# Performance work log

Measured on AMD Instinct MI355X. Metric: run time of the kernel, lower is better.

Reference implementation:

```python
import jax, jax.numpy as jnp
import numpy as np

EPS = 1e-12  # F.normalize default eps


def setup_inputs() -> dict:
    key = jax.random.key(0)
    k1, k2 = jax.random.split(key)
    b, c, angRes, h, w = 4, 64, 5, 64, 64
    d = 64  # dims
    x = jax.random.normal(k1, (b, c, angRes * angRes, h, w), dtype=jnp.float32)
    # 1x1 conv weight [3*dims, channels] (kernel size 1, no bias)
    W = jax.random.normal(k2, (3 * d, c), dtype=jnp.float32) * 0.02
    return {"x": x, "W": W}


def reference(x, W):
    b, c, n, h, w = x.shape
    d = W.shape[0] // 3
    # 1x1 conv over angular (u,v) grid == channel matmul; rearranges are free reindexings
    qkv = jnp.einsum('oc,bcnhw->bonhw', W, x)  # [b, 3d, n, h, w]
    q, k, v = jnp.split(qkv, 3, axis=1)        # each [b, d, n, h, w]

    def flat(t):  # '(b h w) c u v -> b (u v) (c h w)'
        return t.transpose(0, 2, 1, 3, 4).reshape(b, n, d * h * w)

    q, k, v = flat(q), flat(k), flat(v)
    # L2-normalize along the (c h w) feature dim (k was normalized on dim=-2 of its
    # transposed layout, which is this same feature dim)
    q = q / jnp.maximum(jnp.linalg.norm(q, axis=-1, keepdims=True), EPS)
    k = k / jnp.maximum(jnp.linalg.norm(k, axis=-1, keepdims=True), EPS)
    att = jax.nn.softmax(jnp.einsum('bnf,bmf->bnm', q, k), axis=-1)  # [b, n, n], n=25
    out = jnp.einsum('bnm,bmf->bnf', att, v)   # [b, n, d*h*w]
    # 'b (u v) (c h w) -> b c (u v) h w'
    return out.reshape(b, n, d, h, w).transpose(0, 2, 1, 3, 4)
```

## Files before the change

### kernel.cpp

```cpp
#include <hip/hip_runtime.h>

#define B   4
#define C   64
#define D   64
#define NN  25
#define HW  4096
#define F   (D*HW)

#define PT  128
#define QCH 256
#define NCH 4

typedef unsigned short ushort_t;
typedef unsigned int   uint_t;
typedef __attribute__((ext_vector_type(8)))  short  short8;
typedef __attribute__((ext_vector_type(8)))  unsigned short us8;
typedef __attribute__((ext_vector_type(16))) float  floatx16;
typedef __attribute__((ext_vector_type(4)))  float  f32x4;
typedef __attribute__((ext_vector_type(4)))  unsigned short us4;

__device__ ushort_t g_Wthi[128 * C];
__device__ ushort_t g_Wtlo[128 * C];
__device__ ushort_t g_Wvhi[D * C];
__device__ ushort_t g_Wvlo[D * C];

__device__ float g_S[B * NN * NN];
__device__ float g_qq[B * NN];
__device__ float g_kk[B * NN];
__device__ float g_attT[B * NN * NN];

static __device__ __forceinline__ ushort_t f2bf(float f) {
    uint_t u = __float_as_uint(f);
    u += 0x7FFFu + ((u >> 16) & 1u);
    return (ushort_t)(u >> 16);
}
static __device__ __forceinline__ float bf2f(ushort_t h) {
    return __uint_as_float((uint_t)h << 16);
}

static __device__ __forceinline__ int lds_x(int p, int c) {
    return p * 64 + ((((c >> 3) ^ (p & 7)) << 3) | (c & 7));
}

__global__ void k_zero() {
    int i = blockIdx.x * 256 + threadIdx.x;
    if (i < 2500)      g_S[i] = 0.f;
    else if (i < 2600) g_qq[i - 2500] = 0.f;
    else if (i < 2700) g_kk[i - 2600] = 0.f;
}

__global__ void k_wprep(const float* __restrict__ W) {
    int i = blockIdx.x * 256 + threadIdx.x;
    if (i < 128 * 64) {
        float w = W[i];
        ushort_t hi = f2bf(w);
        g_Wthi[i] = hi;
        g_Wtlo[i] = f2bf(w - bf2f(hi));
    } else if (i < 192 * 64) {
        float w = W[i];
        int j = i - 128 * 64;
        ushort_t hi = f2bf(w);
        g_Wvhi[j] = hi;
        g_Wvlo[j] = f2bf(w - bf2f(hi));
    }
}

__global__ void __launch_bounds__(256, 4)
k_proj(const float* __restrict__ x,
       ushort_t* __restrict__ Q, ushort_t* __restrict__ K,
       float* __restrict__ V) {
    __shared__ ushort_t sXhi[PT * 64];
    __shared__ ushort_t sXlo[PT * 64];

    const int t  = threadIdx.x;
    const int wv = t >> 6, ln = t & 63;
    const int n  = blockIdx.y, b = blockIdx.z;
    const int tile = blockIdx.x;
    const int gp0  = tile * PT;

    const int row = ln & 31, kh = (ln >> 5) * 8, d0 = wv * 32;
    short8 ahi[4], alo[4];
#pragma unroll
    for (int ks = 0; ks < 4; ++ks) {
        ahi[ks] = *(const short8*)&g_Wthi[(d0 + row) * 64 + ks * 16 + kh];
        alo[ks] = *(const short8*)&g_Wtlo[(d0 + row) * 64 + ks * 16 + kh];
    }

    {
        const int c16 = wv * 16;
#pragma unroll
        for (int cg = 0; cg < 4; ++cg) {
            const int c4 = c16 + cg * 4;
            const float* xc = x + ((size_t)(b * C + c4) * NN + n) * HW + gp0;
#pragma unroll
            for (int ph = 0; ph < 2; ++ph) {
                const int p = ph * 64 + ln;
                float v[4];
#pragma unroll
                for (int i = 0; i < 4; ++i) v[i] = xc[(size_t)i * NN * HW + p];
                us4 h, l;
#pragma unroll
                for (int i = 0; i < 4; ++i) {
                    ushort_t hi = f2bf(v[i]);
                    h[i] = hi;
                    l[i] = f2bf(v[i] - bf2f(hi));
                }
                *(us4*)&sXhi[lds_x(p, c4)] = h;
                *(us4*)&sXlo[lds_x(p, c4)] = l;
            }
        }
    }
    __syncthreads();

    ushort_t* __restrict__ O = (wv < 2) ? Q : K;
    const int slab = (wv < 2) ? wv : wv - 2;
    const size_t nbase = (size_t)(b * NN + n) * F;

    float nrm = 0.f;
#pragma unroll
    for (int pt = 0; pt < 4; ++pt) {
        const int pcol = pt * 32 + row;
        floatx16 acc;
#pragma unroll
        for (int r = 0; r < 16; ++r) acc[r] = 0.f;
#pragma unroll
        for (int ks = 0; ks < 4; ++ks) {
            const int c0 = ks * 16 + kh;
            short8 bhi = *(const short8*)&sXhi[lds_x(pcol, c0)];
            short8 blo = *(const short8*)&sXlo[lds_x(pcol, c0)];
            acc = __builtin_amdgcn_mfma_f32_32x32x16_bf16(ahi[ks], bhi, acc, 0, 0, 0);
            acc = __builtin_amdgcn_mfma_f32_32x32x16_bf16(alo[ks], bhi, acc, 0, 0, 0);
            acc = __builtin_amdgcn_mfma_f32_32x32x16_bf16(ahi[ks], blo, acc, 0, 0, 0);
        }
#pragma unroll
        for (int r4 = 0; r4 < 4; ++r4) {
            us4 h;
#pragma unroll
            for (int j = 0; j < 4; ++j) {
                const float a = acc[r4 * 4 + j];
                nrm += a * a;
                h[j] = f2bf(a);
            }
            *(us4*)&O[nbase + (((size_t)((tile * 2 + slab) * 16 + pt * 4 + r4)) << 8)
                      + ln * 4] = h;
        }
    }
    for (int off = 32; off > 0; off >>= 1) nrm += __shfl_xor(nrm, off);
    if (ln == 0) atomicAdd(((wv < 2) ? g_qq : g_kk) + b * NN + n, nrm);

    {
        const int sv = wv & 1, ph = wv >> 1;
        short8 vhi[4], vlo[4];
#pragma unroll
        for (int ks = 0; ks < 4; ++ks) {
            vhi[ks] = *(const short8*)&g_Wvhi[(sv * 32 + row) * 64 + ks * 16 + kh];
            vlo[ks] = *(const short8*)&g_Wvlo[(sv * 32 + row) * 64 + ks * 16 + kh];
        }
#pragma unroll
        for (int pt = 0; pt < 2; ++pt) {
            const int pcol = ph * 64 + pt * 32 + row;
            floatx16 acc;
#pragma unroll
            for (int r = 0; r < 16; ++r) acc[r] = 0.f;
#pragma unroll
            for (int ks = 0; ks < 4; ++ks) {
                const int c0 = ks * 16 + kh;
                short8 bhi = *(const short8*)&sXhi[lds_x(pcol, c0)];
                short8 blo = *(const short8*)&sXlo[lds_x(pcol, c0)];
                acc = __builtin_amdgcn_mfma_f32_32x32x16_bf16(vhi[ks], bhi, acc, 0, 0, 0);
                acc = __builtin_amdgcn_mfma_f32_32x32x16_bf16(vlo[ks], bhi, acc, 0, 0, 0);
                acc = __builtin_amdgcn_mfma_f32_32x32x16_bf16(vhi[ks], blo, acc, 0, 0, 0);
            }
#pragma unroll
            for (int r4 = 0; r4 < 4; ++r4) {
                f32x4 o;
#pragma unroll
                for (int j = 0; j < 4; ++j) o[j] = acc[r4 * 4 + j];
                *(f32x4*)&V[nbase + (((size_t)((((tile * 2 + sv) * 2 + ph) * 2 + pt) * 4
                    + r4)) << 8) + ln * 4] = o;
            }
        }
    }
}

__global__ void __launch_bounds__(512, 8)
k_sqk(const ushort_t* __restrict__ Q, const ushort_t* __restrict__ K) {
    __shared__ __align__(16) unsigned char smem[35904];
    ushort_t* sQ = (ushort_t*)smem;
    ushort_t* sK = (ushort_t*)(smem + 16384);
    float (*redS)[64][17] = (float (*)[64][17])smem;

    const int t  = threadIdx.x;
    const int wv = t >> 6, ln = t & 63;
    const int b  = blockIdx.y;
    const size_t fbase = (size_t)blockIdx.x * (QCH * NCH);

    const int col = t & 31;
    const int r0  = t >> 5;
    const int rr  = ln & 31;
    const int khalf = ln >> 5;

    floatx16 acc;
#pragma unroll
    for (int r = 0; r < 16; ++r) acc[r] = 0.f;

    for (int ch = 0; ch < NCH; ++ch) {
        const size_t f0 = fbase + (size_t)ch * QCH;
        if (ch) __syncthreads();
#pragma unroll
        for (int pass = 0; pass < 2; ++pass) {
            const int r  = pass * 16 + r0;
            const int rc = (r < NN) ? r : (NN - 1);
            const size_t g = ((size_t)b * NN + rc) * F + f0 + col * 8;
            const int lx = r * QCH + ((col ^ (r & 7)) * 8);
            *(us8*)&sQ[lx] = *(const us8*)(Q + g);
            *(us8*)&sK[lx] = *(const us8*)(K + g);
        }
        __syncthreads();
#pragma unroll
        for (int i = 0; i < 2; ++i) {
            const int cunit = (wv * 2 + i) * 2 + khalf;
            const int lx = rr * QCH + ((cunit ^ (rr & 7)) * 8);
            short8 aq = *(const short8*)&sQ[lx];
            short8 bk = *(const short8*)&sK[lx];
            acc = __builtin_amdgcn_mfma_f32_32x32x16_bf16(aq, bk, acc, 0, 0, 0);
        }
    }

    __syncthreads();
#pragma unroll
    for (int r = 0; r < 16; ++r) redS[wv][ln][r] = acc[r];
    __syncthreads();
    if (wv == 0) {
#pragma unroll
        for (int r = 0; r < 16; ++r) {
            float v = 0.f;
#pragma unroll
            for (int w = 0; w < 8; ++w) v += redS[w][ln][r];
            const int srow = (r & 3) + 8 * (r >> 2) + 4 * (ln >> 5);
            const int scol = ln & 31;
            if (srow < NN && scol < NN)
                atomicAdd(&g_S[((size_t)b * NN + srow) * NN + scol], v);
        }
    }
}

__global__ void k_softmax() {
    const int b = blockIdx.x, n = threadIdx.x;
    if (n >= NN) return;
    const float qn = fmaxf(sqrtf(g_qq[b * NN + n]), 1e-12f);
    float l[NN], mx = -1e30f;
#pragma unroll
    for (int m = 0; m < NN; ++m) {
        const float km = fmaxf(sqrtf(g_kk[b * NN + m]), 1e-12f);
        l[m] = g_S[((size_t)b * NN + n) * NN + m] / (qn * km);
        mx = fmaxf(mx, l[m]);
    }
    float s = 0.f;
#pragma unroll
    for (int m = 0; m < NN; ++m) { l[m] = expf(l[m] - mx); s += l[m]; }
    const float inv = 1.f / s;
#pragma unroll
    for (int m = 0; m < NN; ++m) g_attT[((size_t)b * NN + m) * NN + n] = l[m] * inv;
}

__global__ void __launch_bounds__(256, 4)
k_outmix(const float* __restrict__ V, float* __restrict__ out) {
    const int tid = blockIdx.x * 256 + threadIdx.x;
    const int b   = blockIdx.y;
    const float* Vb = V + (size_t)b * NN * F + (size_t)tid * 4;
    const float* at = g_attT + b * NN * NN;

    f32x4 acc[NN];
#pragma unroll
    for (int n = 0; n < NN; ++n) acc[n] = 0.f;
#pragma unroll 5
    for (int m = 0; m < NN; ++m) {
        const f32x4 v = *(const f32x4*)(Vb + (size_t)m * F);
#pragma unroll
        for (int n = 0; n < NN; ++n) acc[n] += at[m * NN + n] * v;
    }

    const int ln = tid & 63, c0 = tid >> 6;
    const int r4 = c0 & 3, pt = (c0 >> 2) & 1, ph = (c0 >> 3) & 1;
    const int sv = (c0 >> 4) & 1, tile = c0 >> 5;
    const int p  = tile * 128 + ph * 64 + pt * 32 + (ln & 31);
    const int db = sv * 32 + 8 * r4 + 4 * (ln >> 5);
#pragma unroll
    for (int n = 0; n < NN; ++n)
#pragma unroll
        for (int j = 0; j < 4; ++j)
            out[((size_t)(b * D + db + j) * NN + n) * HW + p] = acc[n][j];
}

extern "C" void kernel_launch(void* const* d_in, const int* in_sizes, int n_in,
                              void* d_out, int out_size, void* d_ws, size_t ws_size,
                              hipStream_t stream) {
    const float* x = (const float*)d_in[0];
    const float* W = (const float*)d_in[1];
    float* outf = (float*)d_out;

    ushort_t* Q = (ushort_t*)d_out;
    ushort_t* K = Q + (size_t)B * NN * F;
    float*    V = (float*)d_ws;

    k_zero   <<<dim3(11),               256, 0, stream>>>();
    k_wprep  <<<dim3(48),               256, 0, stream>>>(W);
    k_proj   <<<dim3(HW/PT, NN, B),     256, 0, stream>>>(x, Q, K, V);
    k_sqk    <<<dim3(F/(QCH*NCH), B),   512, 0, stream>>>(Q, K);
    k_softmax<<<dim3(B),                 64, 0, stream>>>();
    k_outmix <<<dim3(F/1024, B),        256, 0, stream>>>(V, outf);
}
```

Baseline: 302.9 us.

## Load x directly into MFMA operand registers and fuse V projection into QK loop

Removes the shared-memory staging of the bf16 hi/lo split of x in k_proj. Each wave now loads its B operands straight from global memory, converting them in registers. It then reuses those registers for the V projection inside the same pt loop instead of running a separate V pass. The zeroing and weight-prep kernels are also merged into one launch. The cost is that each wave redundantly loads x: four waves read the same columns, and the strided global loads are only 32 floats wide. This relies on cache hits to avoid extra DRAM traffic.

Result: slower. 500.0 us (+65.1%).

```diff
diff --git a/kernel.cpp b/kernel.cpp
--- a/kernel.cpp
+++ b/kernel.cpp
@@ -38,19 +38,11 @@
     return __uint_as_float((uint_t)h << 16);
 }
 
-static __device__ __forceinline__ int lds_x(int p, int c) {
-    return p * 64 + ((((c >> 3) ^ (p & 7)) << 3) | (c & 7));
-}
-
-__global__ void k_zero() {
+__global__ void k_prep(const float* __restrict__ W) {
     int i = blockIdx.x * 256 + threadIdx.x;
     if (i < 2500)      g_S[i] = 0.f;
     else if (i < 2600) g_qq[i - 2500] = 0.f;
     else if (i < 2700) g_kk[i - 2600] = 0.f;
-}
-
-__global__ void k_wprep(const float* __restrict__ W) {
-    int i = blockIdx.x * 256 + threadIdx.x;
     if (i < 128 * 64) {
         float w = W[i];
         ushort_t hi = f2bf(w);
@@ -69,68 +61,56 @@
 k_proj(const float* __restrict__ x,
        ushort_t* __restrict__ Q, ushort_t* __restrict__ K,
        float* __restrict__ V) {
-    __shared__ ushort_t sXhi[PT * 64];
-    __shared__ ushort_t sXlo[PT * 64];
-
     const int t  = threadIdx.x;
     const int wv = t >> 6, ln = t & 63;
     const int n  = blockIdx.y, b = blockIdx.z;
     const int tile = blockIdx.x;
     const int gp0  = tile * PT;
-
-    const int row = ln & 31, kh = (ln >> 5) * 8, d0 = wv * 32;
+    const int row = ln & 31, kh8 = (ln >> 5) * 8;
+    const size_t cstride = (size_t)NN * HW;
+    const float* xp = x + ((size_t)(b * C) * NN + n) * HW + gp0;
+
+    const int d0 = wv * 32;
     short8 ahi[4], alo[4];
 #pragma unroll
     for (int ks = 0; ks < 4; ++ks) {
-        ahi[ks] = *(const short8*)&g_Wthi[(d0 + row) * 64 + ks * 16 + kh];
-        alo[ks] = *(const short8*)&g_Wtlo[(d0 + row) * 64 + ks * 16 + kh];
-    }
-
-    {
-        const int c16 = wv * 16;
-#pragma unroll
-        for (int cg = 0; cg < 4; ++cg) {
-            const int c4 = c16 + cg * 4;
-            const float* xc = x + ((size_t)(b * C + c4) * NN + n) * HW + gp0;
-#pragma unroll
-            for (int ph = 0; ph < 2; ++ph) {
-                const int p = ph * 64 + ln;
-                float v[4];
-#pragma unroll
-                for (int i = 0; i < 4; ++i) v[i] = xc[(size_t)i * NN * HW + p];
-                us4 h, l;
-#pragma unroll
-                for (int i = 0; i < 4; ++i) {
-                    ushort_t hi = f2bf(v[i]);
-                    h[i] = hi;
-                    l[i] = f2bf(v[i] - bf2f(hi));
-                }
-                *(us4*)&sXhi[lds_x(p, c4)] = h;
-                *(us4*)&sXlo[lds_x(p, c4)] = l;
-            }
-        }
-    }
-    __syncthreads();
+        ahi[ks] = *(const short8*)&g_Wthi[(d0 + row) * 64 + ks * 16 + kh8];
+        alo[ks] = *(const short8*)&g_Wtlo[(d0 + row) * 64 + ks * 16 + kh8];
+    }
 
     ushort_t* __restrict__ O = (wv < 2) ? Q : K;
-    const int slab = (wv < 2) ? wv : wv - 2;
+    const int slab = wv & 1;
+    const int sv = wv & 1, ph = wv >> 1;
     const size_t nbase = (size_t)(b * NN + n) * F;
 
     float nrm = 0.f;
 #pragma unroll
     for (int pt = 0; pt < 4; ++pt) {
         const int pcol = pt * 32 + row;
+
+        short8 bhi[4], blo[4];
+#pragma unroll
+        for (int ks = 0; ks < 4; ++ks) {
+            float xv[8];
+#pragma unroll
+            for (int j = 0; j < 8; ++j)
+                xv[j] = xp[(size_t)(ks * 16 + kh8 + j) * cstride + pcol];
+#pragma unroll
+            for (int j = 0; j < 8; ++j) {
+                const ushort_t hi = f2bf(xv[j]);
+                bhi[ks][j] = (short)hi;
+                blo[ks][j] = (short)f2bf(xv[j] - bf2f(hi));
+            }
+        }
+
         floatx16 acc;
 #pragma unroll
         for (int r = 0; r < 16; ++r) acc[r] = 0.f;
 #pragma unroll
         for (int ks = 0; ks < 4; ++ks) {
-            const int c0 = ks * 16 + kh;
-            short8 bhi = *(const short8*)&sXhi[lds_x(pcol, c0)];
-            short8 blo = *(const short8*)&sXlo[lds_x(pcol, c0)];
-            acc = __builtin_amdgcn_mfma_f32_32x32x16_bf16(ahi[ks], bhi, acc, 0, 0, 0);
-            acc = __builtin_amdgcn_mfma_f32_32x32x16_bf16(alo[ks], bhi, acc, 0, 0, 0);
-            acc = __builtin_amdgcn_mfma_f32_32x32x16_bf16(ahi[ks], blo, acc, 0, 0, 0);
+            acc = __builtin_amdgcn_mfma_f32_32x32x16_bf16(ahi[ks], bhi[ks], acc, 0, 0, 0);
+            acc = __builtin_amdgcn_mfma_f32_32x32x16_bf16(alo[ks], bhi[ks], acc, 0, 0, 0);
+            acc = __builtin_amdgcn_mfma_f32_32x32x16_bf16(ahi[ks], blo[ks], acc, 0, 0, 0);
         }
 #pragma unroll
         for (int r4 = 0; r4 < 4; ++r4) {
@@ -144,43 +124,36 @@
             *(us4*)&O[nbase + (((size_t)((tile * 2 + slab) * 16 + pt * 4 + r4)) << 8)
                       + ln * 4] = h;
         }
+
+        if ((pt >> 1) == ph) {
+            const int ptv = pt & 1;
+            short8 vhi[4], vlo[4];
+#pragma unroll
+            for (int ks = 0; ks < 4; ++ks) {
+                vhi[ks] = *(const short8*)&g_Wvhi[(sv * 32 + row) * 64 + ks * 16 + kh8];
+                vlo[ks] = *(const short8*)&g_Wvlo[(sv * 32 + row) * 64 + ks * 16 + kh8];
+            }
+            floatx16 av;
+#pragma unroll
+            for (int r = 0; r < 16; ++r) av[r] = 0.f;
+#pragma unroll
+            for (int ks = 0; ks < 4; ++ks) {
+                av = __builtin_amdgcn_mfma_f32_32x32x16_bf16(vhi[ks], bhi[ks], av, 0, 0, 0);
+                av = __builtin_amdgcn_mfma_f32_32x32x16_bf16(vlo[ks], bhi[ks], av, 0, 0, 0);
+                av = __builtin_amdgcn_mfma_f32_32x32x16_bf16(vhi[ks], blo[ks], av, 0, 0, 0);
+            }
+#pragma unroll
+            for (int r4 = 0; r4 < 4; ++r4) {
+                f32x4 vv;
+#pragma unroll
+                for (int j = 0; j < 4; ++j) vv[j] = av[r4 * 4 + j];
+                *(f32x4*)&V[nbase + (((size_t)((((tile * 2 + sv) * 2 + ph) * 2 + ptv) * 4
+                    + r4)) << 8) + ln * 4] = vv;
+            }
+        }
     }
     for (int off = 32; off > 0; off >>= 1) nrm += __shfl_xor(nrm, off);
     if (ln == 0) atomicAdd(((wv < 2) ? g_qq : g_kk) + b * NN + n, nrm);
-
-    {
-        const int sv = wv & 1, ph = wv >> 1;
-        short8 vhi[4], vlo[4];
-#pragma unroll
-        for (int ks = 0; ks < 4; ++ks) {
-            vhi[ks] = *(const short8*)&g_Wvhi[(sv * 32 + row) * 64 + ks * 16 + kh];
-            vlo[ks] = *(const short8*)&g_Wvlo[(sv * 32 + row) * 64 + ks * 16 + kh];
-        }
-#pragma unroll
-        for (int pt = 0; pt < 2; ++pt) {
-            const int pcol = ph * 64 + pt * 32 + row;
-            floatx16 acc;
-#pragma unroll
-            for (int r = 0; r < 16; ++r) acc[r] = 0.f;
-#pragma unroll
-            for (int ks = 0; ks < 4; ++ks) {
-                const int c0 = ks * 16 + kh;
-                short8 bhi = *(const short8*)&sXhi[lds_x(pcol, c0)];
-                short8 blo = *(const short8*)&sXlo[lds_x(pcol, c0)];
-                acc = __builtin_amdgcn_mfma_f32_32x32x16_bf16(vhi[ks], bhi, acc, 0, 0, 0);
-                acc = __builtin_amdgcn_mfma_f32_32x32x16_bf16(vlo[ks], bhi, acc, 0, 0, 0);
-                acc = __builtin_amdgcn_mfma_f32_32x32x16_bf16(vhi[ks], blo, acc, 0, 0, 0);
-            }
-#pragma unroll
-            for (int r4 = 0; r4 < 4; ++r4) {
-                f32x4 o;
-#pragma unroll
-                for (int j = 0; j < 4; ++j) o[j] = acc[r4 * 4 + j];
-                *(f32x4*)&V[nbase + (((size_t)((((tile * 2 + sv) * 2 + ph) * 2 + pt) * 4
-                    + r4)) << 8) + ln * 4] = o;
-            }
-        }
-    }
 }
 
 __global__ void __launch_bounds__(512, 8)
@@ -282,9 +255,9 @@
     }
 
     const int ln = tid & 63, c0 = tid >> 6;
-    const int r4 = c0 & 3, pt = (c0 >> 2) & 1, ph = (c0 >> 3) & 1;
+    const int r4 = c0 & 3, ptv = (c0 >> 2) & 1, ph = (c0 >> 3) & 1;
     const int sv = (c0 >> 4) & 1, tile = c0 >> 5;
-    const int p  = tile * 128 + ph * 64 + pt * 32 + (ln & 31);
+    const int p  = tile * 128 + ph * 64 + ptv * 32 + (ln & 31);
     const int db = sv * 32 + 8 * r4 + 4 * (ln >> 5);
 #pragma unroll
     for (int n = 0; n < NN; ++n)
@@ -304,8 +277,7 @@
     ushort_t* K = Q + (size_t)B * NN * F;
     float*    V = (float*)d_ws;
 
-    k_zero   <<<dim3(11),               256, 0, stream>>>();
-    k_wprep  <<<dim3(48),               256, 0, stream>>>(W);
+    k_prep   <<<dim3(48),               256, 0, stream>>>(W);
     k_proj   <<<dim3(HW/PT, NN, B),     256, 0, stream>>>(x, Q, K, V);
     k_sqk    <<<dim3(F/(QCH*NCH), B),   512, 0, stream>>>(Q, K);
     k_softmax<<<dim3(B),                 64, 0, stream>>>();
```

## Halve projection pixel tile to 64 and merge zero and weight-prep kernels

Applied to the files above, without the earlier changes.

The projection kernel's pixel tile shrinks from 128 to 64, which doubles the grid and halves per-block work and shared memory. The Q/K/V output index maps and the out-mix kernel's index decoding are rewritten to match the new tile layout. The zeroing and weight-split kernels are merged into one launch to save a kernel dispatch. The aim is more blocks for better occupancy and load balance, at the cost of twice as many weight-fragment loads and norm atomics per pixel.

New measurement: 356.4 us. 1.18x slower.

```diff
diff --git a/kernel.cpp b/kernel.cpp
--- a/kernel.cpp
+++ b/kernel.cpp
@@ -7,7 +7,7 @@
 #define HW  4096
 #define F   (D*HW)
 
-#define PT  128
+#define PT  64
 #define QCH 256
 #define NCH 4
 
@@ -42,15 +42,11 @@
     return p * 64 + ((((c >> 3) ^ (p & 7)) << 3) | (c & 7));
 }
 
-__global__ void k_zero() {
+__global__ void k_prep(const float* __restrict__ W) {
     int i = blockIdx.x * 256 + threadIdx.x;
     if (i < 2500)      g_S[i] = 0.f;
     else if (i < 2600) g_qq[i - 2500] = 0.f;
     else if (i < 2700) g_kk[i - 2600] = 0.f;
-}
-
-__global__ void k_wprep(const float* __restrict__ W) {
-    int i = blockIdx.x * 256 + threadIdx.x;
     if (i < 128 * 64) {
         float w = W[i];
         ushort_t hi = f2bf(w);
@@ -77,13 +73,14 @@
     const int n  = blockIdx.y, b = blockIdx.z;
     const int tile = blockIdx.x;
     const int gp0  = tile * PT;
-
-    const int row = ln & 31, kh = (ln >> 5) * 8, d0 = wv * 32;
+    const size_t cstride = (size_t)NN * HW;
+
+    const int row = ln & 31, kh8 = (ln >> 5) * 8, d0 = wv * 32;
     short8 ahi[4], alo[4];
 #pragma unroll
     for (int ks = 0; ks < 4; ++ks) {
-        ahi[ks] = *(const short8*)&g_Wthi[(d0 + row) * 64 + ks * 16 + kh];
-        alo[ks] = *(const short8*)&g_Wtlo[(d0 + row) * 64 + ks * 16 + kh];
+        ahi[ks] = *(const short8*)&g_Wthi[(d0 + row) * 64 + ks * 16 + kh8];
+        alo[ks] = *(const short8*)&g_Wtlo[(d0 + row) * 64 + ks * 16 + kh8];
     }
 
     {
@@ -92,40 +89,36 @@
         for (int cg = 0; cg < 4; ++cg) {
             const int c4 = c16 + cg * 4;
             const float* xc = x + ((size_t)(b * C + c4) * NN + n) * HW + gp0;
-#pragma unroll
-            for (int ph = 0; ph < 2; ++ph) {
-                const int p = ph * 64 + ln;
-                float v[4];
-#pragma unroll
-                for (int i = 0; i < 4; ++i) v[i] = xc[(size_t)i * NN * HW + p];
-                us4 h, l;
-#pragma unroll
-                for (int i = 0; i < 4; ++i) {
-                    ushort_t hi = f2bf(v[i]);
-                    h[i] = hi;
-                    l[i] = f2bf(v[i] - bf2f(hi));
-                }
-                *(us4*)&sXhi[lds_x(p, c4)] = h;
-                *(us4*)&sXlo[lds_x(p, c4)] = l;
+            float v[4];
+#pragma unroll
+            for (int i = 0; i < 4; ++i) v[i] = xc[(size_t)i * cstride + ln];
+            us4 h, l;
+#pragma unroll
+            for (int i = 0; i < 4; ++i) {
+                ushort_t hi = f2bf(v[i]);
+                h[i] = hi;
+                l[i] = f2bf(v[i] - bf2f(hi));
             }
+            *(us4*)&sXhi[lds_x(ln, c4)] = h;
+            *(us4*)&sXlo[lds_x(ln, c4)] = l;
         }
     }
     __syncthreads();
 
     ushort_t* __restrict__ O = (wv < 2) ? Q : K;
-    const int slab = (wv < 2) ? wv : wv - 2;
+    const int slab = wv & 1;
     const size_t nbase = (size_t)(b * NN + n) * F;
 
     float nrm = 0.f;
 #pragma unroll
-    for (int pt = 0; pt < 4; ++pt) {
+    for (int pt = 0; pt < 2; ++pt) {
         const int pcol = pt * 32 + row;
         floatx16 acc;
 #pragma unroll
         for (int r = 0; r < 16; ++r) acc[r] = 0.f;
 #pragma unroll
         for (int ks = 0; ks < 4; ++ks) {
-            const int c0 = ks * 16 + kh;
+            const int c0 = ks * 16 + kh8;
             short8 bhi = *(const short8*)&sXhi[lds_x(pcol, c0)];
             short8 blo = *(const short8*)&sXlo[lds_x(pcol, c0)];
             acc = __builtin_amdgcn_mfma_f32_32x32x16_bf16(ahi[ks], bhi, acc, 0, 0, 0);
@@ -141,7 +134,7 @@
                 nrm += a * a;
                 h[j] = f2bf(a);
             }
-            *(us4*)&O[nbase + (((size_t)((tile * 2 + slab) * 16 + pt * 4 + r4)) << 8)
+            *(us4*)&O[nbase + (((size_t)((tile * 2 + slab) * 8 + pt * 4 + r4)) << 8)
                       + ln * 4] = h;
         }
     }
@@ -149,36 +142,33 @@
     if (ln == 0) atomicAdd(((wv < 2) ? g_qq : g_kk) + b * NN + n, nrm);
 
     {
-        const int sv = wv & 1, ph = wv >> 1;
+        const int sv = wv & 1, ptv = (wv >> 1) & 1;
         short8 vhi[4], vlo[4];
 #pragma unroll
         for (int ks = 0; ks < 4; ++ks) {
-            vhi[ks] = *(const short8*)&g_Wvhi[(sv * 32 + row) * 64 + ks * 16 + kh];
-            vlo[ks] = *(const short8*)&g_Wvlo[(sv * 32 + row) * 64 + ks * 16 + kh];
-        }
-#pragma unroll
-        for (int pt = 0; pt < 2; ++pt) {
-            const int pcol = ph * 64 + pt * 32 + row;
-            floatx16 acc;
-#pragma unroll
-            for (int r = 0; r < 16; ++r) acc[r] = 0.f;
-#pragma unroll
-            for (int ks = 0; ks < 4; ++ks) {
-                const int c0 = ks * 16 + kh;
-                short8 bhi = *(const short8*)&sXhi[lds_x(pcol, c0)];
-                short8 blo = *(const short8*)&sXlo[lds_x(pcol, c0)];
-                acc = __builtin_amdgcn_mfma_f32_32x32x16_bf16(vhi[ks], bhi, acc, 0, 0, 0);
-                acc = __builtin_amdgcn_mfma_f32_32x32x16_bf16(vlo[ks], bhi, acc, 0, 0, 0);
-                acc = __builtin_amdgcn_mfma_f32_32x32x16_bf16(vhi[ks], blo, acc, 0, 0, 0);
-            }
-#pragma unroll
-            for (int r4 = 0; r4 < 4; ++r4) {
-                f32x4 o;
-#pragma unroll
-                for (int j = 0; j < 4; ++j) o[j] = acc[r4 * 4 + j];
-                *(f32x4*)&V[nbase + (((size_t)((((tile * 2 + sv) * 2 + ph) * 2 + pt) * 4
-                    + r4)) << 8) + ln * 4] = o;
-            }
+            vhi[ks] = *(const short8*)&g_Wvhi[(sv * 32 + row) * 64 + ks * 16 + kh8];
+            vlo[ks] = *(const short8*)&g_Wvlo[(sv * 32 + row) * 64 + ks * 16 + kh8];
+        }
+        const int pcol = ptv * 32 + row;
+        floatx16 av;
+#pragma unroll
+        for (int r = 0; r < 16; ++r) av[r] = 0.f;
+#pragma unroll
+        for (int ks = 0; ks < 4; ++ks) {
+            const int c0 = ks * 16 + kh8;
+            short8 bhi = *(const short8*)&sXhi[lds_x(pcol, c0)];
+            short8 blo = *(const short8*)&sXlo[lds_x(pcol, c0)];
+            av = __builtin_amdgcn_mfma_f32_32x32x16_bf16(vhi[ks], bhi, av, 0, 0, 0);
+            av = __builtin_amdgcn_mfma_f32_32x32x16_bf16(vlo[ks], bhi, av, 0, 0, 0);
+            av = __builtin_amdgcn_mfma_f32_32x32x16_bf16(vhi[ks], blo, av, 0, 0, 0);
+        }
+#pragma unroll
+        for (int r4 = 0; r4 < 4; ++r4) {
+            f32x4 vv;
+#pragma unroll
+            for (int j = 0; j < 4; ++j) vv[j] = av[r4 * 4 + j];
+            *(f32x4*)&V[nbase + (((size_t)((tile * 4 + sv * 2 + ptv) * 4 + r4)) << 8)
+                        + ln * 4] = vv;
         }
     }
 }
@@ -282,9 +272,9 @@
     }
 
     const int ln = tid & 63, c0 = tid >> 6;
-    const int r4 = c0 & 3, pt = (c0 >> 2) & 1, ph = (c0 >> 3) & 1;
-    const int sv = (c0 >> 4) & 1, tile = c0 >> 5;
-    const int p  = tile * 128 + ph * 64 + pt * 32 + (ln & 31);
+    const int r4 = c0 & 3, ptv = (c0 >> 2) & 1, sv = (c0 >> 3) & 1;
+    const int tile = c0 >> 4;
+    const int p  = tile * 64 + ptv * 32 + (ln & 31);
     const int db = sv * 32 + 8 * r4 + 4 * (ln >> 5);
 #pragma unroll
     for (int n = 0; n < NN; ++n)
@@ -304,8 +294,7 @@
     ushort_t* K = Q + (size_t)B * NN * F;
     float*    V = (float*)d_ws;
 
-    k_zero   <<<dim3(11),               256, 0, stream>>>();
-    k_wprep  <<<dim3(48),               256, 0, stream>>>(W);
+    k_prep   <<<dim3(48),               256, 0, stream>>>(W);
     k_proj   <<<dim3(HW/PT, NN, B),     256, 0, stream>>>(x, Q, K, V);
     k_sqk    <<<dim3(F/(QCH*NCH), B),   512, 0, stream>>>(Q, K);
     k_softmax<<<dim3(B),                 64, 0, stream>>>();
```
